# Kernel optimization log

Measured on AMD Instinct MI355X. Metric: run time of the kernel, lower is better.

The kernel has to match this reference:

```python
import jax, jax.numpy as jnp
import numpy as np

N, E, D = 10000, 640000, 128
H1, H2, OUT = 256, 256, 64
EPS = 1e-5

def _layernorm(h, g, b):
    m = jnp.mean(h, axis=-1, keepdims=True)
    v = jnp.mean((h - m) ** 2, axis=-1, keepdims=True)
    return (h - m) * jax.lax.rsqrt(v + EPS) * g + b

def setup_inputs() -> dict:
    key = jax.random.key(0)
    ks = jax.random.split(key, 20)
    def lin(k, fan_in, fan_out):
        bound = 1.0 / np.sqrt(fan_in)
        kw, kb = jax.random.split(k)
        W = jax.random.uniform(kw, (fan_in, fan_out), jnp.float32, -bound, bound)
        b = jax.random.uniform(kb, (fan_out,), jnp.float32, -bound, bound)
        return W, b
    pool_w, pool_b = lin(ks[0], D, D)
    w1, b1 = lin(ks[1], D, H1)
    w2, b2 = lin(ks[2], H1, H2)
    mu_w, mu_b = lin(ks[3], H2, OUT)
    lv_w, lv_b = lin(ks[4], H2, OUT)
    return {
        "x": jax.random.normal(ks[5], (N, D), jnp.float32),
        "edge_index": jax.random.randint(ks[6], (2, E), 0, N, jnp.int32),
        "edge_strength": jax.random.uniform(ks[7], (E,), jnp.float32),
        "ewmc": jnp.float32(0.5),
        "pool_w": pool_w, "pool_b": pool_b,
        "lnp_g": jnp.ones((D,), jnp.float32), "lnp_b": jnp.zeros((D,), jnp.float32),
        "w1": w1, "b1": b1,
        "ln1_g": jnp.ones((H1,), jnp.float32), "ln1_b": jnp.zeros((H1,), jnp.float32),
        "w2": w2, "b2": b2,
        "ln2_g": jnp.ones((H2,), jnp.float32), "ln2_b": jnp.zeros((H2,), jnp.float32),
        "mu_w": mu_w, "mu_b": mu_b,
        "lv_w": lv_w, "lv_b": lv_b,
    }

def reference(x, edge_index, edge_strength, ewmc, pool_w, pool_b, lnp_g, lnp_b,
              w1, b1, ln1_g, ln1_b, w2, b2, ln2_g, ln2_b, mu_w, mu_b, lv_w, lv_b):
    src, dst = edge_index[0], edge_index[1]
    coef = jax.nn.softplus(ewmc)
    # [E, D] gather + edge scaling
    msgs = x[src] * (1.0 + coef * edge_strength[:, None])
    pooled = jax.nn.relu(_layernorm(msgs @ pool_w + pool_b, lnp_g, lnp_b))
    # segment max by dst; torch_scatter fills empty segments with 0 and pooled >= 0
    agg = jax.ops.segment_max(pooled, dst, num_segments=x.shape[0])
    agg = jnp.maximum(agg, 0.0)
    h = jax.nn.relu(_layernorm(agg @ w1 + b1, ln1_g, ln1_b))
    h = jax.nn.relu(_layernorm(h @ w2 + b2, ln2_g, ln2_b))
    mu = h @ mu_w + mu_b
    logvar = h @ lv_w + lv_b
    std = jnp.exp(0.5 * logvar)
    return (mu, std)
```

## Files before the change

### kernel.cpp

```cpp
#include <hip/hip_runtime.h>
#include <math.h>

#define D_DIM   128
#define H1_DIM  256
#define H2_DIM  256
#define OUT_DIM 64
#define LN_EPS  1e-5f
#define NSHARD  4

typedef __attribute__((ext_vector_type(8))) short bf16x8;
typedef __attribute__((ext_vector_type(4))) float f32x4;

__device__ __forceinline__ unsigned short bf16rne(float v) {
    unsigned int b = __float_as_uint(v);
    return (unsigned short)((b + 0x7FFFu + ((b >> 16) & 1u)) >> 16);
}

__global__ __launch_bounds__(128) void k_pool(
        const float* __restrict__ x, const float* __restrict__ pw,
        const float* __restrict__ pb,
        float* __restrict__ y, float4* __restrict__ stat4,
        const int* __restrict__ ei, int* __restrict__ cnt, int E, int epb,
        const float* __restrict__ w1, const float* __restrict__ w2,
        const float* __restrict__ muw, const float* __restrict__ lvw,
        short* __restrict__ wp1, short* __restrict__ wp2,
        short* __restrict__ wpH) {
    __shared__ float xs[8][132];
    __shared__ float ys[8][132];
    __shared__ float pbs[128];
    int tid = threadIdx.x;
    int row0 = blockIdx.x * 8;
    pbs[tid] = pb[tid];
#pragma unroll
    for (int r = 0; r < 8; ++r) xs[r][tid] = x[(row0 + r) * D_DIM + tid];
    {
        int ebeg = blockIdx.x * epb;
        int eend = ebeg + epb; if (eend > E) eend = E;
        for (int e = ebeg + tid; e < eend; e += 128)
            atomicAdd(&cnt[ei[E + e] * NSHARD + (e & (NSHARD - 1))], 1);
    }
    __syncthreads();
    float acc[8];
#pragma unroll
    for (int r = 0; r < 8; ++r) acc[r] = 0.f;
    for (int k = 0; k < D_DIM; k += 4) {
        float wa = pw[k * D_DIM + tid];
        float wb = pw[(k + 1) * D_DIM + tid];
        float wc = pw[(k + 2) * D_DIM + tid];
        float wd = pw[(k + 3) * D_DIM + tid];
#pragma unroll
        for (int r = 0; r < 8; ++r) {
            float4 xv = *(const float4*)&xs[r][k];
            acc[r] = fmaf(xv.x, wa, fmaf(xv.y, wb, fmaf(xv.z, wc, fmaf(xv.w, wd, acc[r]))));
        }
    }
#pragma unroll
    for (int r = 0; r < 8; ++r) {
        y[(row0 + r) * D_DIM + tid] = acc[r];
        ys[r][tid] = acc[r];
    }
    __syncthreads();
    if (tid < 24) {
        int r = tid / 3, which = tid % 3;
        float s = 0.f;
        if (which == 0)      for (int k = 0; k < D_DIM; ++k) s += ys[r][k];
        else if (which == 1) for (int k = 0; k < D_DIM; ++k) s += ys[r][k] * ys[r][k];
        else                 for (int k = 0; k < D_DIM; ++k) s += ys[r][k] * pbs[k];
        s *= (1.f / 128.f);
        ((float*)&stat4[row0 + r])[which] = s;
    }
    if (blockIdx.x < 128) {
        int i = blockIdx.x * 128 + tid;
        const float* W; int Ndim, kt, ln, col; short* dst;
        if (i < 4096) {
            int q = i >> 6; ln = i & 63; kt = q & 3; int ct = q >> 2;
            W = w1; Ndim = H1_DIM; col = ct * 16 + (ln & 15); dst = wp1 + i * 8;
        } else if (i < 12288) {
            int i2 = i - 4096; int q = i2 >> 6; ln = i2 & 63; kt = q & 7; int ct = q >> 3;
            W = w2; Ndim = H2_DIM; col = ct * 16 + (ln & 15); dst = wp2 + i2 * 8;
        } else {
            int i3 = i - 12288; int q = i3 >> 6; ln = i3 & 63; kt = q & 7; int ct = q >> 3;
            Ndim = OUT_DIM; dst = wpH + i3 * 8;
            if (ct < 4) { W = muw; col = ct * 16 + (ln & 15); }
            else        { W = lvw; col = (ct - 4) * 16 + (ln & 15); }
        }
        int k0 = kt * 32 + (ln >> 4) * 8;
        unsigned int u[4];
#pragma unroll
        for (int jj = 0; jj < 4; ++jj) {
            float a = W[(k0 + 2 * jj) * Ndim + col];
            float b = W[(k0 + 2 * jj + 1) * Ndim + col];
            u[jj] = (unsigned int)bf16rne(a) | ((unsigned int)bf16rne(b) << 16);
        }
        *(uint4*)dst = make_uint4(u[0], u[1], u[2], u[3]);
    }
}

__global__ __launch_bounds__(1024) void k_scanA(
        const int* __restrict__ cnt, int* __restrict__ offs,
        int* __restrict__ bsum, int N4) {
    __shared__ int part[1024];
    const int t = threadIdx.x;
    const int idx = blockIdx.x * 1024 + t;
    int v = (idx < N4) ? cnt[idx] : 0;
    part[t] = v;
    __syncthreads();
    for (int off = 1; off < 1024; off <<= 1) {
        int n = (t >= off) ? part[t - off] : 0;
        __syncthreads();
        part[t] += n;
        __syncthreads();
    }
    if (idx < N4) offs[idx] = part[t] - v;
    if (t == 1023) bsum[blockIdx.x] = part[t];
}

__global__ __launch_bounds__(64) void k_scanB(
        const int* __restrict__ bsum, int* __restrict__ bbase,
        int* __restrict__ offs, float* __restrict__ consts,
        const float* __restrict__ ewmc, const float* __restrict__ pb,
        int nblk, int N4) {
    const int l = threadIdx.x;
    {
        float v0 = pb[l], v1 = pb[l + 64];
        float s1 = v0 + v1, s2 = v0 * v0 + v1 * v1;
#pragma unroll
        for (int off = 1; off < 64; off <<= 1) {
            s1 += __shfl_xor(s1, off, 64);
            s2 += __shfl_xor(s2, off, 64);
        }
        if (l == 0) {
            float xw = ewmc[0];
            consts[0] = (xw > 30.f) ? xw : log1pf(expf(xw));
            consts[1] = s1 * (1.f / 128.f);
            consts[2] = s2 * (1.f / 128.f);
        }
    }
    int val = (l < nblk) ? bsum[l] : 0;
    int orig = val;
#pragma unroll
    for (int off = 1; off < 64; off <<= 1) {
        int n = __shfl_up(val, off, 64);
        if (l >= off) val += n;
    }
    if (l < nblk) bbase[l] = val - orig;
    if (l == nblk - 1) offs[N4] = val;
}

__global__ __launch_bounds__(1024) void k_scanC(
        int* __restrict__ offs, int* __restrict__ head,
        const int* __restrict__ bbase, int N4) {
    int idx = blockIdx.x * 1024 + threadIdx.x;
    if (idx < N4) {
        int o = offs[idx] + bbase[blockIdx.x];
        offs[idx] = o;
        head[idx] = o;
    }
}

__global__ __launch_bounds__(256) void k_scatter(
        const int* __restrict__ ei, const float* __restrict__ es,
        const float* __restrict__ consts, const float4* __restrict__ stat4,
        int* __restrict__ head, float4* __restrict__ pairs, int E) {
    const float coef = consts[0], mpb = consts[1], mpb2 = consts[2];
    const int tid = threadIdx.x;
    const int e0 = blockIdx.x * 1024 + tid;
    int srcv[4], dstv[4]; float sv[4]; float4 st[4]; int pos[4]; bool ok[4];
#pragma unroll
    for (int u = 0; u < 4; ++u) {
        int e = e0 + u * 256;
        ok[u] = (e < E);
        if (ok[u]) { srcv[u] = ei[e]; dstv[u] = ei[E + e]; sv[u] = es[e]; }
    }
#pragma unroll
    for (int u = 0; u < 4; ++u) if (ok[u]) st[u] = stat4[srcv[u]];
#pragma unroll
    for (int u = 0; u < 4; ++u) if (ok[u]) {
        int e = e0 + u * 256;
        pos[u] = atomicAdd(&head[dstv[u] * NSHARD + (e & (NSHARD - 1))], 1);
    }
#pragma unroll
    for (int u = 0; u < 4; ++u) if (ok[u]) {
        float s = fmaf(coef, sv[u], 1.0f);
        float m   = fmaf(s, st[u].x, mpb);
        float et2 = fmaf(s * s, st[u].y, fmaf(2.f * s, st[u].z, mpb2));
        float inv = rsqrtf(et2 - m * m + LN_EPS);
        pairs[pos[u]] = make_float4(__int_as_float(srcv[u]), s, m, inv);
    }
}

__global__ __launch_bounds__(256) void k_gather(
        const float4* __restrict__ pairs, const int* __restrict__ offs,
        const float* __restrict__ y, const float* __restrict__ pb,
        const float* __restrict__ g, const float* __restrict__ b,
        float* __restrict__ agg, int N) {
    const int node = blockIdx.x * 4 + (threadIdx.x >> 6);
    if (node >= N) return;
    const int lane = threadIdx.x & 63;
    const int sub  = lane >> 5;
    const int q    = lane & 31;
    const int d0   = q * 4;
    const float4 pbv = *(const float4*)&pb[d0];
    const float4 gv  = *(const float4*)&g[d0];
    const float4 bv  = *(const float4*)&b[d0];
    float4 mx = make_float4(-INFINITY, -INFINITY, -INFINITY, -INFINITY);
    int j = offs[node * NSHARD];
    const int end = offs[node * NSHARD + NSHARD];
    for (; j + 12 <= end; j += 12) {
        float4 p[6], yv[6];
#pragma unroll
        for (int u = 0; u < 6; ++u) p[u] = pairs[j + 2 * u + sub];
#pragma unroll
        for (int u = 0; u < 6; ++u)
            yv[u] = *(const float4*)&y[(size_t)__float_as_int(p[u].x) * D_DIM + d0];
#pragma unroll
        for (int u = 0; u < 6; ++u) {
            float s = p[u].y, m = p[u].z, inv = p[u].w;
            mx.x = fmaxf(mx.x, fmaf(fmaf(s, yv[u].x, pbv.x) - m, inv * gv.x, bv.x));
            mx.y = fmaxf(mx.y, fmaf(fmaf(s, yv[u].y, pbv.y) - m, inv * gv.y, bv.y));
            mx.z = fmaxf(mx.z, fmaf(fmaf(s, yv[u].z, pbv.z) - m, inv * gv.z, bv.z));
            mx.w = fmaxf(mx.w, fmaf(fmaf(s, yv[u].w, pbv.w) - m, inv * gv.w, bv.w));
        }
    }
    for (; j + 2 <= end; j += 2) {
        float4 p = pairs[j + sub];
        float4 yv = *(const float4*)&y[(size_t)__float_as_int(p.x) * D_DIM + d0];
        float s = p.y, m = p.z, inv = p.w;
        mx.x = fmaxf(mx.x, fmaf(fmaf(s, yv.x, pbv.x) - m, inv * gv.x, bv.x));
        mx.y = fmaxf(mx.y, fmaf(fmaf(s, yv.y, pbv.y) - m, inv * gv.y, bv.y));
        mx.z = fmaxf(mx.z, fmaf(fmaf(s, yv.z, pbv.z) - m, inv * gv.z, bv.z));
        mx.w = fmaxf(mx.w, fmaf(fmaf(s, yv.w, pbv.w) - m, inv * gv.w, bv.w));
    }
    if (j < end) {
        float4 p = pairs[j];
        float4 yv = *(const float4*)&y[(size_t)__float_as_int(p.x) * D_DIM + d0];
        float s = p.y, m = p.z, inv = p.w;
        mx.x = fmaxf(mx.x, fmaf(fmaf(s, yv.x, pbv.x) - m, inv * gv.x, bv.x));
        mx.y = fmaxf(mx.y, fmaf(fmaf(s, yv.y, pbv.y) - m, inv * gv.y, bv.y));
        mx.z = fmaxf(mx.z, fmaf(fmaf(s, yv.z, pbv.z) - m, inv * gv.z, bv.z));
        mx.w = fmaxf(mx.w, fmaf(fmaf(s, yv.w, pbv.w) - m, inv * gv.w, bv.w));
    }
    mx.x = fmaxf(mx.x, __shfl_xor(mx.x, 32, 64));
    mx.y = fmaxf(mx.y, __shfl_xor(mx.y, 32, 64));
    mx.z = fmaxf(mx.z, __shfl_xor(mx.z, 32, 64));
    mx.w = fmaxf(mx.w, __shfl_xor(mx.w, 32, 64));
    if (sub == 0) {
        float4 o;
        o.x = fmaxf(mx.x, 0.f); o.y = fmaxf(mx.y, 0.f);
        o.z = fmaxf(mx.z, 0.f); o.w = fmaxf(mx.w, 0.f);
        *(float4*)&agg[node * D_DIM + d0] = o;
    }
}

__global__ __launch_bounds__(512) void k_mlp(
        const float* __restrict__ agg,
        const short* __restrict__ wp1, const short* __restrict__ wp2,
        const short* __restrict__ wpH,
        const float* __restrict__ b1, const float* __restrict__ g1,
        const float* __restrict__ bb1,
        const float* __restrict__ b2, const float* __restrict__ g2,
        const float* __restrict__ bb2,
        const float* __restrict__ mub, const float* __restrict__ lvb,
        float* __restrict__ out, int N) {
    __shared__ __align__(16) short aPack[8 * 64 * 8];
    __shared__ float sPart[16][8][2];
    __shared__ float sM[16], sI[16];
    const int tid  = threadIdx.x;
    const int w    = tid >> 6;
    const int lane = tid & 63;
    const int gq   = lane >> 4;
    const int c16  = lane & 15;
    const int row0 = blockIdx.x * 16;

    {
        int r  = tid >> 5;
        int k0 = (tid & 31) * 4;
        float4 v = *(const float4*)&agg[(size_t)(row0 + r) * D_DIM + k0];
        int kt = k0 >> 5, sub = (k0 >> 3) & 3, j = k0 & 7;
        int lp = r | (sub << 4);
        unsigned int u0 = (unsigned int)bf16rne(v.x) | ((unsigned int)bf16rne(v.y) << 16);
        unsigned int u1 = (unsigned int)bf16rne(v.z) | ((unsigned int)bf16rne(v.w) << 16);
        *(uint2*)&aPack[kt * 512 + lp * 8 + j] = make_uint2(u0, u1);
    }
    __syncthreads();

    const int ct0 = 2 * w, ct1 = 2 * w + 1;
    f32x4 A0 = {0.f, 0.f, 0.f, 0.f}, A1 = {0.f, 0.f, 0.f, 0.f};

#pragma unroll
    for (int kt = 0; kt < 4; ++kt) {
        bf16x8 av = *(bf16x8*)&aPack[(kt * 64 + lane) * 8];
        bf16x8 bv0 = *(const bf16x8*)&wp1[((ct0 * 4 + kt) * 64 + lane) * 8];
        bf16x8 bv1 = *(const bf16x8*)&wp1[((ct1 * 4 + kt) * 64 + lane) * 8];
        A0 = __builtin_amdgcn_mfma_f32_16x16x32_bf16(av, bv0, A0, 0, 0, 0);
        A1 = __builtin_amdgcn_mfma_f32_16x16x32_bf16(av, bv1, A1, 0, 0, 0);
    }
    {
        int col0 = ct0 * 16 + c16, col1 = ct1 * 16 + c16;
        float bias0 = b1[col0], bias1 = b1[col1];
        float v0[4], v1[4];
#pragma unroll
        for (int r = 0; r < 4; ++r) {
            v0[r] = A0[r] + bias0; v1[r] = A1[r] + bias1;
            float s1 = v0[r] + v1[r];
            float s2 = v0[r] * v0[r] + v1[r] * v1[r];
#pragma unroll
            for (int m = 1; m < 16; m <<= 1) {
                s1 += __shfl_xor(s1, m, 64);
                s2 += __shfl_xor(s2, m, 64);
            }
            if (c16 == 0) { sPart[gq * 4 + r][w][0] = s1; sPart[gq * 4 + r][w][1] = s2; }
        }
        __syncthreads();
        if (tid < 16) {
            float t1 = 0.f, t2 = 0.f;
#pragma unroll
            for (int ww = 0; ww < 8; ++ww) { t1 += sPart[tid][ww][0]; t2 += sPart[tid][ww][1]; }
            float m = t1 * (1.f / 256.f);
            sM[tid] = m;
            sI[tid] = rsqrtf(t2 * (1.f / 256.f) - m * m + LN_EPS);
        }
        __syncthreads();
        float gc0 = g1[col0], bc0 = bb1[col0];
        float gc1 = g1[col1], bc1 = bb1[col1];
#pragma unroll
        for (int r = 0; r < 4; ++r) {
            int row = gq * 4 + r;
            float m = sM[row], inv = sI[row];
            float h0 = fmaxf(fmaf((v0[r] - m) * inv, gc0, bc0), 0.f);
            float h1 = fmaxf(fmaf((v1[r] - m) * inv, gc1, bc1), 0.f);
            aPack[(col0 >> 5) * 512 + (row | (((col0 >> 3) & 3) << 4)) * 8 + (col0 & 7)] = (short)bf16rne(h0);
            aPack[(col1 >> 5) * 512 + (row | (((col1 >> 3) & 3) << 4)) * 8 + (col1 & 7)] = (short)bf16rne(h1);
        }
    }
    __syncthreads();

    A0 = (f32x4){0.f, 0.f, 0.f, 0.f}; A1 = (f32x4){0.f, 0.f, 0.f, 0.f};
#pragma unroll
    for (int kt = 0; kt < 8; ++kt) {
        bf16x8 av = *(bf16x8*)&aPack[(kt * 64 + lane) * 8];
        bf16x8 bv0 = *(const bf16x8*)&wp2[((ct0 * 8 + kt) * 64 + lane) * 8];
        bf16x8 bv1 = *(const bf16x8*)&wp2[((ct1 * 8 + kt) * 64 + lane) * 8];
        A0 = __builtin_amdgcn_mfma_f32_16x16x32_bf16(av, bv0, A0, 0, 0, 0);
        A1 = __builtin_amdgcn_mfma_f32_16x16x32_bf16(av, bv1, A1, 0, 0, 0);
    }
    {
        int col0 = ct0 * 16 + c16, col1 = ct1 * 16 + c16;
        float bias0 = b2[col0], bias1 = b2[col1];
        float v0[4], v1[4];
#pragma unroll
        for (int r = 0; r < 4; ++r) {
            v0[r] = A0[r] + bias0; v1[r] = A1[r] + bias1;
            float s1 = v0[r] + v1[r];
            float s2 = v0[r] * v0[r] + v1[r] * v1[r];
#pragma unroll
            for (int m = 1; m < 16; m <<= 1) {
                s1 += __shfl_xor(s1, m, 64);
                s2 += __shfl_xor(s2, m, 64);
            }
            if (c16 == 0) { sPart[gq * 4 + r][w][0] = s1; sPart[gq * 4 + r][w][1] = s2; }
        }
        __syncthreads();
        if (tid < 16) {
            float t1 = 0.f, t2 = 0.f;
#pragma unroll
            for (int ww = 0; ww < 8; ++ww) { t1 += sPart[tid][ww][0]; t2 += sPart[tid][ww][1]; }
            float m = t1 * (1.f / 256.f);
            sM[tid] = m;
            sI[tid] = rsqrtf(t2 * (1.f / 256.f) - m * m + LN_EPS);
        }
        __syncthreads();
        float gc0 = g2[col0], bc0 = bb2[col0];
        float gc1 = g2[col1], bc1 = bb2[col1];
#pragma unroll
        for (int r = 0; r < 4; ++r) {
            int row = gq * 4 + r;
            float m = sM[row], inv = sI[row];
            float h0 = fmaxf(fmaf((v0[r] - m) * inv, gc0, bc0), 0.f);
            float h1 = fmaxf(fmaf((v1[r] - m) * inv, gc1, bc1), 0.f);
            aPack[(col0 >> 5) * 512 + (row | (((col0 >> 3) & 3) << 4)) * 8 + (col0 & 7)] = (short)bf16rne(h0);
            aPack[(col1 >> 5) * 512 + (row | (((col1 >> 3) & 3) << 4)) * 8 + (col1 & 7)] = (short)bf16rne(h1);
        }
    }
    __syncthreads();

    {
        f32x4 H = {0.f, 0.f, 0.f, 0.f};
#pragma unroll
        for (int kt = 0; kt < 8; ++kt) {
            bf16x8 av = *(bf16x8*)&aPack[(kt * 64 + lane) * 8];
            bf16x8 bv = *(const bf16x8*)&wpH[((w * 8 + kt) * 64 + lane) * 8];
            H = __builtin_amdgcn_mfma_f32_16x16x32_bf16(av, bv, H, 0, 0, 0);
        }
        int colh = (w & 3) * 16 + c16;
        if (w < 4) {
            float bias = mub[colh];
#pragma unroll
            for (int r = 0; r < 4; ++r)
                out[(size_t)(row0 + gq * 4 + r) * OUT_DIM + colh] = H[r] + bias;
        } else {
            float bias = lvb[colh];
#pragma unroll
            for (int r = 0; r < 4; ++r)
                out[(size_t)N * OUT_DIM + (size_t)(row0 + gq * 4 + r) * OUT_DIM + colh] =
                    expf(0.5f * (H[r] + bias));
        }
    }
}

extern "C" void kernel_launch(void* const* d_in, const int* in_sizes, int n_in,
                              void* d_out, int out_size, void* d_ws, size_t ws_size,
                              hipStream_t stream) {
    const float* x      = (const float*)d_in[0];
    const int*   ei     = (const int*)  d_in[1];
    const float* es     = (const float*)d_in[2];
    const float* ewmc   = (const float*)d_in[3];
    const float* pool_w = (const float*)d_in[4];
    const float* pool_b = (const float*)d_in[5];
    const float* lnp_g  = (const float*)d_in[6];
    const float* lnp_b  = (const float*)d_in[7];
    const float* w1     = (const float*)d_in[8];
    const float* b1     = (const float*)d_in[9];
    const float* ln1_g  = (const float*)d_in[10];
    const float* ln1_b  = (const float*)d_in[11];
    const float* w2     = (const float*)d_in[12];
    const float* b2     = (const float*)d_in[13];
    const float* ln2_g  = (const float*)d_in[14];
    const float* ln2_b  = (const float*)d_in[15];
    const float* mu_w   = (const float*)d_in[16];
    const float* mu_b   = (const float*)d_in[17];
    const float* lv_w   = (const float*)d_in[18];
    const float* lv_b   = (const float*)d_in[19];

    const int N  = in_sizes[0] / D_DIM;
    const int E  = in_sizes[2];
    const int N4 = N * NSHARD;
    const int nblkScan = (N4 + 1023) / 1024;

    float*  ws     = (float*)d_ws;
    float*  consts = ws;
    float4* stat4  = (float4*)(ws + 16);
    float*  y      = ws + 16 + 4 * (size_t)N;
    float*  agg    = y + (size_t)N * D_DIM;
    size_t  w      = 16 + 4 * (size_t)N + 2 * (size_t)N * D_DIM;
    int*    cnt    = (int*)(ws + w); w += N4;
    int*    offs   = (int*)(ws + w); w += N4 + 1;
    int*    head   = (int*)(ws + w); w += N4;
    int*    bsum   = (int*)(ws + w); w += 64;
    int*    bbase  = (int*)(ws + w); w += 64;
    w = (w + 3) & ~(size_t)3;
    short*  wp1    = (short*)(ws + w); w += 16384;
    short*  wp2    = (short*)(ws + w); w += 32768;
    short*  wpH    = (short*)(ws + w); w += 16384;
    float4* pairs  = (float4*)(ws + w);

    const int nb  = N / 8;
    const int epb = (E + nb - 1) / nb;

    hipMemsetAsync(cnt, 0, (size_t)N4 * sizeof(int), stream);
    k_pool<<<nb, 128, 0, stream>>>(x, pool_w, pool_b, y, stat4, ei, cnt, E, epb,
                                   w1, w2, mu_w, lv_w, wp1, wp2, wpH);
    k_scanA<<<nblkScan, 1024, 0, stream>>>(cnt, offs, bsum, N4);
    k_scanB<<<1, 64, 0, stream>>>(bsum, bbase, offs, consts, ewmc, pool_b,
                                  nblkScan, N4);
    k_scanC<<<nblkScan, 1024, 0, stream>>>(offs, head, bbase, N4);
    k_scatter<<<(E + 1023) / 1024, 256, 0, stream>>>(ei, es, consts, stat4,
                                                     head, pairs, E);
    k_gather<<<(N + 3) / 4, 256, 0, stream>>>(pairs, offs, y,
                                              pool_b, lnp_g, lnp_b, agg, N);
    k_mlp<<<N / 16, 512, 0, stream>>>(agg, wp1, wp2, wpH,
                                      b1, ln1_g, ln1_b,
                                      b2, ln2_g, ln2_b,
                                      mu_b, lv_b, (float*)d_out, N);
}
```

Baseline: 138.6 us.

## Compute pooling projection with bf16 MFMA and store it as bf16 for gather

Replaces the scalar FP32 pooling matmul with a bf16 16x16x32 MFMA over 16-row tiles in 512-thread blocks. Per-row LayerNorm statistics are now computed with wave shuffles on the rounded values. The intermediate y is stored as bf16, halving the bytes read per edge in the gather kernel, which now handles 8 features per lane and 4 edges per wave step. This trades accuracy (x, pool_w and y all rounded to bf16) for less memory traffic in the bandwidth-bound gather and less ALU work in the projection.

New measurement: 118.5 us. 14.5% less time.

```diff
diff --git a/kernel.cpp b/kernel.cpp
--- a/kernel.cpp
+++ b/kernel.cpp
@@ -16,61 +16,107 @@
     return (unsigned short)((b + 0x7FFFu + ((b >> 16) & 1u)) >> 16);
 }
 
-__global__ __launch_bounds__(128) void k_pool(
+union BFPack { unsigned int u[4]; bf16x8 v; };
+
+__global__ __launch_bounds__(512) void k_pool(
         const float* __restrict__ x, const float* __restrict__ pw,
         const float* __restrict__ pb,
-        float* __restrict__ y, float4* __restrict__ stat4,
+        unsigned short* __restrict__ y, float4* __restrict__ stat4,
         const int* __restrict__ ei, int* __restrict__ cnt, int E, int epb,
         const float* __restrict__ w1, const float* __restrict__ w2,
         const float* __restrict__ muw, const float* __restrict__ lvw,
         short* __restrict__ wp1, short* __restrict__ wp2,
         short* __restrict__ wpH) {
-    __shared__ float xs[8][132];
-    __shared__ float ys[8][132];
-    __shared__ float pbs[128];
-    int tid = threadIdx.x;
-    int row0 = blockIdx.x * 8;
-    pbs[tid] = pb[tid];
-#pragma unroll
-    for (int r = 0; r < 8; ++r) xs[r][tid] = x[(row0 + r) * D_DIM + tid];
+    __shared__ __align__(16) short aPack[4 * 64 * 8];
+    __shared__ unsigned short yLds[16][128];
+    __shared__ float sPart[16][8][3];
+    const int tid  = threadIdx.x;
+    const int w    = tid >> 6;
+    const int lane = tid & 63;
+    const int gq   = lane >> 4;
+    const int c16  = lane & 15;
+    const int row0 = blockIdx.x * 16;
+
+    bf16x8 bfrag[4];
+    {
+        const int col = w * 16 + c16;
+        const int kbase = gq * 8;
+#pragma unroll
+        for (int kt = 0; kt < 4; ++kt) {
+            int k0 = kt * 32 + kbase;
+            BFPack t;
+#pragma unroll
+            for (int jj = 0; jj < 4; ++jj) {
+                float a = pw[(k0 + 2 * jj) * D_DIM + col];
+                float b = pw[(k0 + 2 * jj + 1) * D_DIM + col];
+                t.u[jj] = (unsigned int)bf16rne(a) | ((unsigned int)bf16rne(b) << 16);
+            }
+            bfrag[kt] = t.v;
+        }
+    }
     {
         int ebeg = blockIdx.x * epb;
         int eend = ebeg + epb; if (eend > E) eend = E;
-        for (int e = ebeg + tid; e < eend; e += 128)
+        for (int e = ebeg + tid; e < eend; e += 512)
             atomicAdd(&cnt[ei[E + e] * NSHARD + (e & (NSHARD - 1))], 1);
     }
+    {
+        int r  = tid >> 5;
+        int k0 = (tid & 31) * 4;
+        float4 v = *(const float4*)&x[(size_t)(row0 + r) * D_DIM + k0];
+        int kt = k0 >> 5, sub = (k0 >> 3) & 3, j = k0 & 7;
+        int lp = r | (sub << 4);
+        unsigned int u0 = (unsigned int)bf16rne(v.x) | ((unsigned int)bf16rne(v.y) << 16);
+        unsigned int u1 = (unsigned int)bf16rne(v.z) | ((unsigned int)bf16rne(v.w) << 16);
+        *(uint2*)&aPack[kt * 512 + lp * 8 + j] = make_uint2(u0, u1);
+    }
     __syncthreads();
-    float acc[8];
-#pragma unroll
-    for (int r = 0; r < 8; ++r) acc[r] = 0.f;
-    for (int k = 0; k < D_DIM; k += 4) {
-        float wa = pw[k * D_DIM + tid];
-        float wb = pw[(k + 1) * D_DIM + tid];
-        float wc = pw[(k + 2) * D_DIM + tid];
-        float wd = pw[(k + 3) * D_DIM + tid];
-#pragma unroll
-        for (int r = 0; r < 8; ++r) {
-            float4 xv = *(const float4*)&xs[r][k];
-            acc[r] = fmaf(xv.x, wa, fmaf(xv.y, wb, fmaf(xv.z, wc, fmaf(xv.w, wd, acc[r]))));
-        }
-    }
-#pragma unroll
-    for (int r = 0; r < 8; ++r) {
-        y[(row0 + r) * D_DIM + tid] = acc[r];
-        ys[r][tid] = acc[r];
+
+    f32x4 A = {0.f, 0.f, 0.f, 0.f};
+#pragma unroll
+    for (int kt = 0; kt < 4; ++kt) {
+        bf16x8 av = *(bf16x8*)&aPack[(kt * 64 + lane) * 8];
+        A = __builtin_amdgcn_mfma_f32_16x16x32_bf16(av, bfrag[kt], A, 0, 0, 0);
+    }
+
+    {
+        float pbf = pb[w * 16 + c16];
+#pragma unroll
+        for (int r = 0; r < 4; ++r) {
+            unsigned short h = bf16rne(A[r]);
+            yLds[gq * 4 + r][w * 16 + c16] = h;
+            float hf = __uint_as_float((unsigned int)h << 16);
+            float s1 = hf, s2 = hf * hf, s3 = hf * pbf;
+#pragma unroll
+            for (int m = 1; m < 16; m <<= 1) {
+                s1 += __shfl_xor(s1, m, 64);
+                s2 += __shfl_xor(s2, m, 64);
+                s3 += __shfl_xor(s3, m, 64);
+            }
+            if (c16 == 0) {
+                sPart[gq * 4 + r][w][0] = s1;
+                sPart[gq * 4 + r][w][1] = s2;
+                sPart[gq * 4 + r][w][2] = s3;
+            }
+        }
     }
     __syncthreads();
-    if (tid < 24) {
-        int r = tid / 3, which = tid % 3;
-        float s = 0.f;
-        if (which == 0)      for (int k = 0; k < D_DIM; ++k) s += ys[r][k];
-        else if (which == 1) for (int k = 0; k < D_DIM; ++k) s += ys[r][k] * ys[r][k];
-        else                 for (int k = 0; k < D_DIM; ++k) s += ys[r][k] * pbs[k];
-        s *= (1.f / 128.f);
-        ((float*)&stat4[row0 + r])[which] = s;
-    }
-    if (blockIdx.x < 128) {
-        int i = blockIdx.x * 128 + tid;
+    {
+        int idx = tid * 4;
+        int r = idx >> 7, c = idx & 127;
+        *(uint2*)&y[(size_t)(row0 + r) * D_DIM + c] = *(const uint2*)&yLds[r][c];
+    }
+    if (tid < 16) {
+        float t1 = 0.f, t2 = 0.f, t3 = 0.f;
+#pragma unroll
+        for (int ww = 0; ww < 8; ++ww) {
+            t1 += sPart[tid][ww][0]; t2 += sPart[tid][ww][1]; t3 += sPart[tid][ww][2];
+        }
+        stat4[row0 + tid] = make_float4(t1 * (1.f / 128.f), t2 * (1.f / 128.f),
+                                        t3 * (1.f / 128.f), 0.f);
+    }
+    if (blockIdx.x < 32) {
+        int i = blockIdx.x * 512 + tid;
         const float* W; int Ndim, kt, ln, col; short* dst;
         if (i < 4096) {
             int q = i >> 6; ln = i & 63; kt = q & 3; int ct = q >> 2;
@@ -189,66 +235,90 @@
     }
 }
 
+#define GPROC(P, YB)                                                          \
+    {                                                                         \
+        float s = (P).y, m = (P).z, inv = (P).w;                              \
+        float y0 = __uint_as_float((YB).x << 16);                             \
+        float y1 = __uint_as_float((YB).x & 0xFFFF0000u);                     \
+        float y2 = __uint_as_float((YB).y << 16);                             \
+        float y3 = __uint_as_float((YB).y & 0xFFFF0000u);                     \
+        float y4 = __uint_as_float((YB).z << 16);                             \
+        float y5 = __uint_as_float((YB).z & 0xFFFF0000u);                     \
+        float y6 = __uint_as_float((YB).w << 16);                             \
+        float y7 = __uint_as_float((YB).w & 0xFFFF0000u);                     \
+        mxA.x = fmaxf(mxA.x, fmaf(fmaf(s, y0, pbA.x) - m, inv * gA.x, bA.x)); \
+        mxA.y = fmaxf(mxA.y, fmaf(fmaf(s, y1, pbA.y) - m, inv * gA.y, bA.y)); \
+        mxA.z = fmaxf(mxA.z, fmaf(fmaf(s, y2, pbA.z) - m, inv * gA.z, bA.z)); \
+        mxA.w = fmaxf(mxA.w, fmaf(fmaf(s, y3, pbA.w) - m, inv * gA.w, bA.w)); \
+        mxB.x = fmaxf(mxB.x, fmaf(fmaf(s, y4, pbB.x) - m, inv * gB.x, bB.x)); \
+        mxB.y = fmaxf(mxB.y, fmaf(fmaf(s, y5, pbB.y) - m, inv * gB.y, bB.y)); \
+        mxB.z = fmaxf(mxB.z, fmaf(fmaf(s, y6, pbB.z) - m, inv * gB.z, bB.z)); \
+        mxB.w = fmaxf(mxB.w, fmaf(fmaf(s, y7, pbB.w) - m, inv * gB.w, bB.w)); \
+    }
+
 __global__ __launch_bounds__(256) void k_gather(
         const float4* __restrict__ pairs, const int* __restrict__ offs,
-        const float* __restrict__ y, const float* __restrict__ pb,
+        const unsigned short* __restrict__ y, const float* __restrict__ pb,
         const float* __restrict__ g, const float* __restrict__ b,
         float* __restrict__ agg, int N) {
     const int node = blockIdx.x * 4 + (threadIdx.x >> 6);
     if (node >= N) return;
     const int lane = threadIdx.x & 63;
-    const int sub  = lane >> 5;
-    const int q    = lane & 31;
-    const int d0   = q * 4;
-    const float4 pbv = *(const float4*)&pb[d0];
-    const float4 gv  = *(const float4*)&g[d0];
-    const float4 bv  = *(const float4*)&b[d0];
-    float4 mx = make_float4(-INFINITY, -INFINITY, -INFINITY, -INFINITY);
+    const int sub  = lane >> 4;
+    const int q    = lane & 15;
+    const int d0   = q * 8;
+    const float4 pbA = *(const float4*)&pb[d0], pbB = *(const float4*)&pb[d0 + 4];
+    const float4 gA  = *(const float4*)&g[d0],  gB  = *(const float4*)&g[d0 + 4];
+    const float4 bA  = *(const float4*)&b[d0],  bB  = *(const float4*)&b[d0 + 4];
+    float4 mxA = make_float4(-INFINITY, -INFINITY, -INFINITY, -INFINITY);
+    float4 mxB = mxA;
     int j = offs[node * NSHARD];
     const int end = offs[node * NSHARD + NSHARD];
     for (; j + 12 <= end; j += 12) {
-        float4 p[6], yv[6];
-#pragma unroll
-        for (int u = 0; u < 6; ++u) p[u] = pairs[j + 2 * u + sub];
-#pragma unroll
-        for (int u = 0; u < 6; ++u)
-            yv[u] = *(const float4*)&y[(size_t)__float_as_int(p[u].x) * D_DIM + d0];
-#pragma unroll
-        for (int u = 0; u < 6; ++u) {
-            float s = p[u].y, m = p[u].z, inv = p[u].w;
-            mx.x = fmaxf(mx.x, fmaf(fmaf(s, yv[u].x, pbv.x) - m, inv * gv.x, bv.x));
-            mx.y = fmaxf(mx.y, fmaf(fmaf(s, yv[u].y, pbv.y) - m, inv * gv.y, bv.y));
-            mx.z = fmaxf(mx.z, fmaf(fmaf(s, yv[u].z, pbv.z) - m, inv * gv.z, bv.z));
-            mx.w = fmaxf(mx.w, fmaf(fmaf(s, yv[u].w, pbv.w) - m, inv * gv.w, bv.w));
-        }
-    }
-    for (; j + 2 <= end; j += 2) {
+        float4 p[3]; uint4 yb[3];
+#pragma unroll
+        for (int u = 0; u < 3; ++u) p[u] = pairs[j + 4 * u + sub];
+#pragma unroll
+        for (int u = 0; u < 3; ++u)
+            yb[u] = *(const uint4*)&y[(size_t)__float_as_int(p[u].x) * D_DIM + d0];
+#pragma unroll
+        for (int u = 0; u < 3; ++u) GPROC(p[u], yb[u]);
+    }
+    for (; j + 4 <= end; j += 4) {
         float4 p = pairs[j + sub];
-        float4 yv = *(const float4*)&y[(size_t)__float_as_int(p.x) * D_DIM + d0];
-        float s = p.y, m = p.z, inv = p.w;
-        mx.x = fmaxf(mx.x, fmaf(fmaf(s, yv.x, pbv.x) - m, inv * gv.x, bv.x));
-        mx.y = fmaxf(mx.y, fmaf(fmaf(s, yv.y, pbv.y) - m, inv * gv.y, bv.y));
-        mx.z = fmaxf(mx.z, fmaf(fmaf(s, yv.z, pbv.z) - m, inv * gv.z, bv.z));
-        mx.w = fmaxf(mx.w, fmaf(fmaf(s, yv.w, pbv.w) - m, inv * gv.w, bv.w));
+        uint4 yb = *(const uint4*)&y[(size_t)__float_as_int(p.x) * D_DIM + d0];
+        GPROC(p, yb);
     }
     if (j < end) {
-        float4 p = pairs[j];
-        float4 yv = *(const float4*)&y[(size_t)__float_as_int(p.x) * D_DIM + d0];
-        float s = p.y, m = p.z, inv = p.w;
-        mx.x = fmaxf(mx.x, fmaf(fmaf(s, yv.x, pbv.x) - m, inv * gv.x, bv.x));
-        mx.y = fmaxf(mx.y, fmaf(fmaf(s, yv.y, pbv.y) - m, inv * gv.y, bv.y));
-        mx.z = fmaxf(mx.z, fmaf(fmaf(s, yv.z, pbv.z) - m, inv * gv.z, bv.z));
-        mx.w = fmaxf(mx.w, fmaf(fmaf(s, yv.w, pbv.w) - m, inv * gv.w, bv.w));
-    }
-    mx.x = fmaxf(mx.x, __shfl_xor(mx.x, 32, 64));
-    mx.y = fmaxf(mx.y, __shfl_xor(mx.y, 32, 64));
-    mx.z = fmaxf(mx.z, __shfl_xor(mx.z, 32, 64));
-    mx.w = fmaxf(mx.w, __shfl_xor(mx.w, 32, 64));
+        int rem = end - j;
+        float4 p = pairs[j + (sub < rem ? sub : 0)];
+        uint4 yb = *(const uint4*)&y[(size_t)__float_as_int(p.x) * D_DIM + d0];
+        GPROC(p, yb);
+    }
+    mxA.x = fmaxf(mxA.x, __shfl_xor(mxA.x, 16, 64));
+    mxA.y = fmaxf(mxA.y, __shfl_xor(mxA.y, 16, 64));
+    mxA.z = fmaxf(mxA.z, __shfl_xor(mxA.z, 16, 64));
+    mxA.w = fmaxf(mxA.w, __shfl_xor(mxA.w, 16, 64));
+    mxB.x = fmaxf(mxB.x, __shfl_xor(mxB.x, 16, 64));
+    mxB.y = fmaxf(mxB.y, __shfl_xor(mxB.y, 16, 64));
+    mxB.z = fmaxf(mxB.z, __shfl_xor(mxB.z, 16, 64));
+    mxB.w = fmaxf(mxB.w, __shfl_xor(mxB.w, 16, 64));
+    mxA.x = fmaxf(mxA.x, __shfl_xor(mxA.x, 32, 64));
+    mxA.y = fmaxf(mxA.y, __shfl_xor(mxA.y, 32, 64));
+    mxA.z = fmaxf(mxA.z, __shfl_xor(mxA.z, 32, 64));
+    mxA.w = fmaxf(mxA.w, __shfl_xor(mxA.w, 32, 64));
+    mxB.x = fmaxf(mxB.x, __shfl_xor(mxB.x, 32, 64));
+    mxB.y = fmaxf(mxB.y, __shfl_xor(mxB.y, 32, 64));
+    mxB.z = fmaxf(mxB.z, __shfl_xor(mxB.z, 32, 64));
+    mxB.w = fmaxf(mxB.w, __shfl_xor(mxB.w, 32, 64));
     if (sub == 0) {
-        float4 o;
-        o.x = fmaxf(mx.x, 0.f); o.y = fmaxf(mx.y, 0.f);
-        o.z = fmaxf(mx.z, 0.f); o.w = fmaxf(mx.w, 0.f);
-        *(float4*)&agg[node * D_DIM + d0] = o;
+        float4 oA, oB;
+        oA.x = fmaxf(mxA.x, 0.f); oA.y = fmaxf(mxA.y, 0.f);
+        oA.z = fmaxf(mxA.z, 0.f); oA.w = fmaxf(mxA.w, 0.f);
+        oB.x = fmaxf(mxB.x, 0.f); oB.y = fmaxf(mxB.y, 0.f);
+        oB.z = fmaxf(mxB.z, 0.f); oB.w = fmaxf(mxB.w, 0.f);
+        *(float4*)&agg[(size_t)node * D_DIM + d0]     = oA;
+        *(float4*)&agg[(size_t)node * D_DIM + d0 + 4] = oB;
     }
 }
 
@@ -440,9 +510,9 @@
     float*  ws     = (float*)d_ws;
     float*  consts = ws;
     float4* stat4  = (float4*)(ws + 16);
-    float*  y      = ws + 16 + 4 * (size_t)N;
-    float*  agg    = y + (size_t)N * D_DIM;
-    size_t  w      = 16 + 4 * (size_t)N + 2 * (size_t)N * D_DIM;
+    unsigned short* y = (unsigned short*)(ws + 16 + 4 * (size_t)N);
+    float*  agg    = ws + 16 + 4 * (size_t)N + (size_t)N * D_DIM / 2;
+    size_t  w      = 16 + 4 * (size_t)N + (size_t)N * D_DIM / 2 + (size_t)N * D_DIM;
     int*    cnt    = (int*)(ws + w); w += N4;
     int*    offs   = (int*)(ws + w); w += N4 + 1;
     int*    head   = (int*)(ws + w); w += N4;
@@ -454,12 +524,12 @@
     short*  wpH    = (short*)(ws + w); w += 16384;
     float4* pairs  = (float4*)(ws + w);
 
-    const int nb  = N / 8;
-    const int epb = (E + nb - 1) / nb;
+    const int nbPool = N / 16;
+    const int epb    = (E + nbPool - 1) / nbPool;
 
     hipMemsetAsync(cnt, 0, (size_t)N4 * sizeof(int), stream);
-    k_pool<<<nb, 128, 0, stream>>>(x, pool_w, pool_b, y, stat4, ei, cnt, E, epb,
-                                   w1, w2, mu_w, lv_w, wp1, wp2, wpH);
+    k_pool<<<nbPool, 512, 0, stream>>>(x, pool_w, pool_b, y, stat4, ei, cnt, E,
+                                       epb, w1, w2, mu_w, lv_w, wp1, wp2, wpH);
     k_scanA<<<nblkScan, 1024, 0, stream>>>(cnt, offs, bsum, N4);
     k_scanB<<<1, 64, 0, stream>>>(bsum, bbase, offs, consts, ewmc, pool_b,
                                   nblkScan, N4);
```
